# Performance work log

Measured on AMD Instinct MI355X. Metric: run time of the kernel, lower is better.

Reference implementation:

```python
import jax, jax.numpy as jnp
import numpy as np

N_NODES = 50000   # field_size == number of graph nodes
N_EDGES = 800000  # avg degree 16
VOCAB = 200000    # feature_size
EMB = 64          # embedding_size == in_dim
HID = 64          # num_hidden
SLOPE = 0.2       # leaky relu negative slope


def setup_inputs() -> dict:
    key = jax.random.key(0)
    ks = jax.random.split(key, 20)
    s = 0.05
    d = {}
    d["features"] = jax.random.randint(ks[0], (8, N_NODES), 0, VOCAB, dtype=jnp.int32)
    d["feature_values"] = jax.random.uniform(ks[1], (8, N_NODES), dtype=jnp.float32)
    d["src"] = jax.random.randint(ks[2], (N_EDGES,), 0, N_NODES, dtype=jnp.int32)
    d["dst"] = jax.random.randint(ks[3], (N_EDGES,), 0, N_NODES, dtype=jnp.int32)
    d["emb"] = jax.random.normal(ks[4], (VOCAB, EMB), jnp.float32) * s
    # layer 0: in=64 -> heads=2, out=64 (no residual)
    d["W0"]  = jax.random.normal(ks[5], (EMB, 2 * HID), jnp.float32) * s
    d["al0"] = jax.random.normal(ks[6], (2, HID), jnp.float32) * s
    d["ar0"] = jax.random.normal(ks[7], (2, HID), jnp.float32) * s
    d["b0"]  = jnp.zeros((2 * HID,), jnp.float32)
    # layer 1: in=128 -> heads=2, out=64 (identity residual since in == heads*out)
    d["W1"]  = jax.random.normal(ks[8], (2 * HID, 2 * HID), jnp.float32) * s
    d["al1"] = jax.random.normal(ks[9], (2, HID), jnp.float32) * s
    d["ar1"] = jax.random.normal(ks[10], (2, HID), jnp.float32) * s
    d["b1"]  = jnp.zeros((2 * HID,), jnp.float32)
    # output layer: in=128 -> heads=1, out=64 (projected residual), no activation
    d["W2"]    = jax.random.normal(ks[11], (2 * HID, EMB), jnp.float32) * s
    d["al2"]   = jax.random.normal(ks[12], (1, EMB), jnp.float32) * s
    d["ar2"]   = jax.random.normal(ks[13], (1, EMB), jnp.float32) * s
    d["b2"]    = jnp.zeros((EMB,), jnp.float32)
    d["resW2"] = jax.random.normal(ks[14], (2 * HID, EMB), jnp.float32) * s
    return d


def _gat_layer(h, src, dst, W, al, ar, b, res, act):
    """DGL-style GATConv. h: [N, in], W: [in, H*D], al/ar: [H, D]."""
    N = h.shape[0]
    H, D = al.shape
    fh = (h @ W).reshape(N, H, D)                      # [N, H, D]
    el = jnp.einsum('nhd,hd->nh', fh, al)              # [N, H]
    er = jnp.einsum('nhd,hd->nh', fh, ar)              # [N, H]
    e = jax.nn.leaky_relu(el[src] + er[dst], SLOPE)    # [E, H]
    # edge softmax grouped by destination node
    m = jax.ops.segment_max(e, dst, num_segments=N)
    m = jnp.where(jnp.isfinite(m), m, 0.0)
    ex = jnp.exp(e - m[dst])
    den = jax.ops.segment_sum(ex, dst, num_segments=N)
    alpha = ex / jnp.maximum(den[dst], 1e-9)           # [E, H]
    out = jax.ops.segment_sum(alpha[:, :, None] * fh[src], dst, num_segments=N)  # [N, H, D]
    if res is not None:
        out = out + res
    out = out + b.reshape(H, D)
    if act:
        out = jax.nn.elu(out)
    return out


def reference(features, feature_values, src, dst, emb,
              W0, al0, ar0, b0, W1, al1, ar1, b1,
              W2, al2, ar2, b2, resW2):
    # embedding lookup scaled by feature values: [B, field, emb]
    fe = emb[features] * feature_values[..., None]
    h = fe[0]                                          # [N_NODES, EMB]
    # layer 0: no residual, elu, flatten heads
    h = _gat_layer(h, src, dst, W0, al0, ar0, b0, None, True).reshape(N_NODES, -1)
    # layer 1: identity residual (in == heads*out), elu, flatten heads
    res1 = h.reshape(N_NODES, 2, HID)
    h = _gat_layer(h, src, dst, W1, al1, ar1, b1, res1, True).reshape(N_NODES, -1)
    # output layer: projected residual, no activation, mean over heads
    res2 = (h @ resW2).reshape(N_NODES, 1, EMB)
    logits = _gat_layer(h, src, dst, W2, al2, ar2, b2, res2, False).mean(axis=1)
    return logits
```

## Files before the change

kernel.cpp:

```cpp
#include <hip/hip_runtime.h>


typedef __attribute__((ext_vector_type(8))) short short8;
typedef __attribute__((ext_vector_type(4))) float float4v;

__device__ __forceinline__ float lrelu(float x){ return x >= 0.f ? x : 0.2f*x; }

__device__ __forceinline__ unsigned short f2bf(float f){
  unsigned int u = __float_as_uint(f);
  u += 0x7fffu + ((u >> 16) & 1u);
  return (unsigned short)(u >> 16);
}
__device__ __forceinline__ float bf2f(unsigned short u){
  return __uint_as_float((unsigned int)u << 16);
}
__device__ __forceinline__ float rl_f(float v, int l){
  return __int_as_float(__builtin_amdgcn_readlane(__float_as_int(v), l));
}

__global__ void k_zero_i32(int* __restrict__ p, int n){
  int i = blockIdx.x*blockDim.x + threadIdx.x;
  if (i < n) p[i] = 0;
}

__global__ void k_hist(const int* __restrict__ dst, int* __restrict__ counts, int E){
  int i = blockIdx.x*blockDim.x + threadIdx.x;
  if (i < E) atomicAdd(&counts[dst[i]], 1);
}

__global__ void k_scan_local(const int* __restrict__ counts, int* __restrict__ row_ptr,
                             int* __restrict__ bsum, int N){
  __shared__ int s[256];
  int t = threadIdx.x, g = blockIdx.x*256 + t;
  int v = (g < N) ? counts[g] : 0;
  s[t] = v; __syncthreads();
  #pragma unroll
  for (int off = 1; off < 256; off <<= 1){
    int x = 0;
    if (t >= off) x = s[t-off];
    __syncthreads();
    s[t] += x;
    __syncthreads();
  }
  if (g < N) row_ptr[g+1] = s[t];
  if (g == 0 && t == 0) row_ptr[0] = 0;
  if (t == 255) bsum[blockIdx.x] = s[255];
}

__global__ void k_scan_top(int* __restrict__ bsum, int nb){
  __shared__ int s[256];
  int t = threadIdx.x;
  int v = (t < nb) ? bsum[t] : 0;
  s[t] = v; __syncthreads();
  #pragma unroll
  for (int off = 1; off < 256; off <<= 1){
    int x = 0;
    if (t >= off) x = s[t-off];
    __syncthreads();
    s[t] += x;
    __syncthreads();
  }
  if (t < nb) bsum[t] = s[t] - v;
}

__global__ void k_scan_fix(int* __restrict__ row_ptr, const int* __restrict__ bsum, int N){
  int g = blockIdx.x*256 + threadIdx.x;
  if (g < N && blockIdx.x > 0) row_ptr[g+1] += bsum[blockIdx.x];
}

__global__ void k_scatter(const int* __restrict__ src, const int* __restrict__ dst,
                          const int* __restrict__ row_ptr, int* __restrict__ cursor,
                          int* __restrict__ ssrc, int E){
  int i = blockIdx.x*blockDim.x + threadIdx.x;
  if (i >= E) return;
  int d = dst[i];
  int pos = atomicAdd(&cursor[d], 1);
  ssrc[row_ptr[d] + pos] = src[i];
}

__global__ void k_wprep(const float* __restrict__ Wa, const float* __restrict__ Wb,
                        int IN, unsigned short* __restrict__ Wt){
  int id = blockIdx.x*256 + threadIdx.x;
  if (id >= 128*IN) return;
  int n = id / IN, k = id % IN;
  float v;
  if (Wb) v = (n < 64) ? Wa[k*64 + n] : Wb[k*64 + (n - 64)];
  else    v = Wa[k*128 + n];
  Wt[n*IN + k] = f2bf(v);
}

__global__ void k_embed(const int* __restrict__ feat, const float* __restrict__ fv,
                        const float* __restrict__ emb, unsigned int* __restrict__ h0b, int N){
  int t = blockIdx.x*blockDim.x + threadIdx.x;
  int n = t >> 4, c4 = t & 15;
  if (n >= N) return;
  float4 v = ((const float4*)(emb + (size_t)feat[n]*64))[c4];
  float sc = fv[n];
  unsigned int p0 = (unsigned)f2bf(v.x*sc) | ((unsigned)f2bf(v.y*sc) << 16);
  unsigned int p1 = (unsigned)f2bf(v.z*sc) | ((unsigned)f2bf(v.w*sc) << 16);
  h0b[(size_t)n*32 + c4*2]     = p0;
  h0b[(size_t)n*32 + c4*2 + 1] = p1;
}

template<int IN, int H>
__global__ __launch_bounds__(256) void k_gemm_mfma(
    const unsigned short* __restrict__ hb,
    const unsigned short* __restrict__ Wt,
    const float* __restrict__ al, const float* __restrict__ ar,
    unsigned short* __restrict__ fhb,
    float* __restrict__ elr, int N){
  constexpr int KS = IN/32;
  constexpr int LDP = IN + 8;
  __shared__ unsigned short Wt_s[128*LDP];
  const int t = threadIdx.x;
  const int lane = t & 63, wid = t >> 6;
  const int l15 = lane & 15, quad = lane >> 4;
  const int row0 = blockIdx.x*64 + wid*16;

  for (int id = t; id < 128*(IN/8); id += 256){
    int r = id/(IN/8), seg = id%(IN/8);
    ((uint4*)(Wt_s + r*LDP))[seg] = ((const uint4*)(Wt + (size_t)r*IN))[seg];
  }
  short8 a[KS];
  int arow = row0 + l15;
  #pragma unroll
  for (int s = 0; s < KS; s++){
    if (arow < N) a[s] = *(const short8*)(hb + (size_t)arow*IN + s*32 + quad*8);
    else          a[s] = short8{0,0,0,0,0,0,0,0};
  }
  __syncthreads();

  float4v acc[8];
  #pragma unroll
  for (int nt = 0; nt < 8; nt++) acc[nt] = float4v{0.f,0.f,0.f,0.f};
  #pragma unroll
  for (int nt = 0; nt < 8; nt++){
    #pragma unroll
    for (int s = 0; s < KS; s++){
      short8 b = *(const short8*)(Wt_s + (nt*16 + l15)*LDP + s*32 + quad*8);
      acc[nt] = __builtin_amdgcn_mfma_f32_16x16x32_bf16(a[s], b, acc[nt], 0, 0, 0);
    }
  }

  float alc[8], arc[8];
  #pragma unroll
  for (int nt = 0; nt < 8; nt++){
    bool hv = (H == 2) || (nt < 4);
    alc[nt] = hv ? al[nt*16 + l15] : 0.f;
    arc[nt] = hv ? ar[nt*16 + l15] : 0.f;
  }
  #pragma unroll
  for (int reg = 0; reg < 4; reg++){
    int row = row0 + quad*4 + reg;
    bool rv = row < N;
    if (rv){
      #pragma unroll
      for (int nt = 0; nt < 8; nt++)
        fhb[(size_t)row*128 + nt*16 + l15] = f2bf(acc[nt][reg]);
    }
    float pel0 = 0.f, per0 = 0.f, pel1 = 0.f, per1 = 0.f;
    #pragma unroll
    for (int nt = 0; nt < 4; nt++){
      pel0 += acc[nt][reg]*alc[nt];     per0 += acc[nt][reg]*arc[nt];
      pel1 += acc[nt+4][reg]*alc[nt+4]; per1 += acc[nt+4][reg]*arc[nt+4];
    }
    #pragma unroll
    for (int off = 1; off < 16; off <<= 1){
      pel0 += __shfl_xor(pel0, off, 64);
      pel1 += __shfl_xor(pel1, off, 64);
      per0 += __shfl_xor(per0, off, 64);
      per1 += __shfl_xor(per1, off, 64);
    }
    if (l15 == 0 && rv){
      elr[row*4+0] = pel0;
      elr[row*4+1] = (H == 2) ? pel1 : 0.f;
      elr[row*4+2] = per0;
      elr[row*4+3] = (H == 2) ? per1 : 0.f;
    }
  }
}

template<int H>
__global__ __launch_bounds__(256) void k_agg(
    const unsigned* __restrict__ fhb, const float* __restrict__ elr,
    const int* __restrict__ row_ptr, const int* __restrict__ ssrc,
    const float* __restrict__ bias, const float* __restrict__ res,
    int act, int res_from_fh,
    float* __restrict__ out, int out_ld, unsigned* __restrict__ outb, int N){
  int lane = threadIdx.x & 63, wid = threadIdx.x >> 6;
  int n = blockIdx.x*4 + wid;
  if (n >= N) return;
  int beg = row_ptr[n], end = row_ptr[n+1];
  float er0 = elr[n*4+2];
  float er1 = (H == 2) ? elr[n*4+3] : 0.f;

  float x0 = 0.f, x1 = 0.f;
  {
    int i = beg + lane;
    if (i < end){
      int s = ssrc[i];
      float2 el = *(const float2*)(elr + s*4);
      x0 = __expf(fminf(lrelu(el.x + er0), 30.f));
      if (H == 2) x1 = __expf(fminf(lrelu(el.y + er1), 30.f));
    }
  }
  float d0 = x0, d1 = x1;
  for (int i = beg + lane + 64; i < end; i += 64){
    int s = ssrc[i];
    float2 el = *(const float2*)(elr + s*4);
    d0 += __expf(fminf(lrelu(el.x + er0), 30.f));
    if (H == 2) d1 += __expf(fminf(lrelu(el.y + er1), 30.f));
  }
  #pragma unroll
  for (int off = 32; off >= 1; off >>= 1){
    d0 += __shfl_xor(d0, off, 64);
    if (H == 2) d1 += __shfl_xor(d1, off, 64);
  }
  float rd0 = d0 > 0.f ? 1.f/d0 : 0.f;
  float rd1 = (H == 2 && d1 > 0.f) ? 1.f/d1 : 0.f;

  float ax = 0.f, ay = 0.f;
  for (int base = beg; base < end; base += 64){
    int i = base + lane;
    int s = 0; float a0 = 0.f, a1 = 0.f;
    if (i < end){
      s = ssrc[i];
      if (base == beg){
        a0 = x0 * rd0; if (H == 2) a1 = x1 * rd1;
      } else {
        float2 el = *(const float2*)(elr + s*4);
        a0 = __expf(fminf(lrelu(el.x + er0), 30.f)) * rd0;
        if (H == 2) a1 = __expf(fminf(lrelu(el.y + er1), 30.f)) * rd1;
      }
    }
    int cnt  = min(64, end - base);
    int cnt8 = (cnt + 7) & ~7;
    if (H == 2){
      for (int j0 = 0; j0 < cnt8; j0 += 8){
        unsigned w[8]; float aj[8];
        #pragma unroll
        for (int u = 0; u < 8; u++){
          int sj = __builtin_amdgcn_readlane(s, j0 + u);
          w[u] = fhb[(size_t)sj*64 + lane];
        }
        #pragma unroll
        for (int u = 0; u < 8; u++){
          float aj0 = rl_f(a0, j0 + u);
          float aj1 = rl_f(a1, j0 + u);
          aj[u] = (lane < 32) ? aj0 : aj1;
        }
        #pragma unroll
        for (int u = 0; u < 8; u++){
          ax += bf2f((unsigned short)(w[u] & 0xffffu)) * aj[u];
          ay += bf2f((unsigned short)(w[u] >> 16))     * aj[u];
        }
      }
    } else {
      const unsigned short* fh16 = (const unsigned short*)fhb;
      for (int j0 = 0; j0 < cnt8; j0 += 8){
        unsigned short w[8]; float aj[8];
        #pragma unroll
        for (int u = 0; u < 8; u++){
          int sj = __builtin_amdgcn_readlane(s, j0 + u);
          w[u] = fh16[(size_t)sj*128 + lane];
        }
        #pragma unroll
        for (int u = 0; u < 8; u++) aj[u] = rl_f(a0, j0 + u);
        #pragma unroll
        for (int u = 0; u < 8; u++) ax += bf2f(w[u]) * aj[u];
      }
    }
  }
  if (H == 2){
    int c0 = lane*2;
    float o0 = ax + bias[c0], o1 = ay + bias[c0+1];
    if (res){ o0 += res[n*128 + c0]; o1 += res[n*128 + c0+1]; }
    if (act){ o0 = o0 > 0.f ? o0 : expm1f(o0); o1 = o1 > 0.f ? o1 : expm1f(o1); }
    *(float2*)(out + n*out_ld + c0) = make_float2(o0, o1);
    if (outb) outb[(size_t)n*64 + lane] = (unsigned)f2bf(o0) | ((unsigned)f2bf(o1) << 16);
  } else {
    const unsigned short* fh16 = (const unsigned short*)fhb;
    float o = ax + bias[lane];
    if (res_from_fh) o += bf2f(fh16[(size_t)n*128 + 64 + lane]);
    out[n*out_ld + lane] = o;
  }
}

extern "C" void kernel_launch(void* const* d_in, const int* in_sizes, int n_in,
                              void* d_out, int out_size, void* d_ws, size_t ws_size,
                              hipStream_t stream) {
  const int*   feat = (const int*)  d_in[0];
  const float* fv   = (const float*)d_in[1];
  const int*   src  = (const int*)  d_in[2];
  const int*   dst  = (const int*)  d_in[3];
  const float* emb  = (const float*)d_in[4];
  const float* W0   = (const float*)d_in[5];
  const float* al0  = (const float*)d_in[6];
  const float* ar0  = (const float*)d_in[7];
  const float* b0   = (const float*)d_in[8];
  const float* W1   = (const float*)d_in[9];
  const float* al1  = (const float*)d_in[10];
  const float* ar1  = (const float*)d_in[11];
  const float* b1   = (const float*)d_in[12];
  const float* W2   = (const float*)d_in[13];
  const float* al2  = (const float*)d_in[14];
  const float* ar2  = (const float*)d_in[15];
  const float* b2   = (const float*)d_in[16];
  const float* rW2  = (const float*)d_in[17];
  const int N = in_sizes[0] / 8;
  const int E = in_sizes[2];

  size_t off = 0;
  auto alloc = [&](size_t bytes) -> void* {
    void* p = (char*)d_ws + off;
    off = (off + bytes + 255) & ~(size_t)255;
    return p;
  };
  unsigned short* P1 = (unsigned short*)alloc((size_t)N*128*sizeof(unsigned short));
  float* P2     = (float*)alloc((size_t)N*128*sizeof(float));
  float* P3     = (float*)alloc((size_t)N*128*sizeof(float));
  unsigned short* hb = (unsigned short*)alloc((size_t)N*128*sizeof(unsigned short));
  float* elr    = (float*)alloc((size_t)N*4*sizeof(float));
  int* row_ptr  = (int*)alloc((size_t)(N+1)*sizeof(int));
  int* counts   = (int*)alloc((size_t)2*N*sizeof(int));
  int* cursor   = counts + N;
  int* ssrc     = (int*)alloc((size_t)E*sizeof(int));
  int* bsum     = (int*)alloc(256*sizeof(int));
  unsigned short* Wt0 = (unsigned short*)alloc((size_t)128*64*sizeof(unsigned short));
  unsigned short* Wt1 = (unsigned short*)alloc((size_t)128*128*sizeof(unsigned short));
  unsigned short* Wt2 = (unsigned short*)alloc((size_t)128*128*sizeof(unsigned short));

  int nb1 = (N + 255) / 256;
  k_zero_i32<<<(2*N + 255)/256, 256, 0, stream>>>(counts, 2*N);
  k_hist<<<(E + 255)/256, 256, 0, stream>>>(dst, counts, E);
  k_scan_local<<<nb1, 256, 0, stream>>>(counts, row_ptr, bsum, N);
  k_scan_top<<<1, 256, 0, stream>>>(bsum, nb1);
  k_scan_fix<<<nb1, 256, 0, stream>>>(row_ptr, bsum, N);
  k_scatter<<<(E + 255)/256, 256, 0, stream>>>(src, dst, row_ptr, cursor, ssrc, E);
  k_wprep<<<(128*64 + 255)/256, 256, 0, stream>>>(W0, nullptr, 64, Wt0);
  k_wprep<<<(128*128 + 255)/256, 256, 0, stream>>>(W1, nullptr, 128, Wt1);
  k_wprep<<<(128*128 + 255)/256, 256, 0, stream>>>(W2, rW2, 128, Wt2);
  k_embed<<<(N*16 + 255)/256, 256, 0, stream>>>(feat, fv, emb, (unsigned int*)hb, N);

  int gt = (N + 63)/64;
  int nagg = (N + 3)/4;
  k_gemm_mfma<64,2><<<gt, 256, 0, stream>>>(hb, Wt0, al0, ar0, P1, elr, N);
  k_agg<2><<<nagg, 256, 0, stream>>>((unsigned*)P1, elr, row_ptr, ssrc, b0, nullptr,
                                     1, 0, P2, 128, (unsigned*)hb, N);
  k_gemm_mfma<128,2><<<gt, 256, 0, stream>>>(hb, Wt1, al1, ar1, P1, elr, N);
  k_agg<2><<<nagg, 256, 0, stream>>>((unsigned*)P1, elr, row_ptr, ssrc, b1, P2,
                                     1, 0, P3, 128, (unsigned*)hb, N);
  k_gemm_mfma<128,1><<<gt, 256, 0, stream>>>(hb, Wt2, al2, ar2, P1, elr, N);
  k_agg<1><<<nagg, 256, 0, stream>>>((unsigned*)P1, elr, row_ptr, ssrc, b2, nullptr,
                                     0, 1, (float*)d_out, 64, nullptr, N);
}
```

Baseline: 368.3 us.

## Record atomic ranks during histogram, merge weight prep, use bpermute for attention broadcast

The histogram kernel now stores each edge's atomic rank, so the scatter pass indexes directly and needs no second set of atomics or cursor array. The three weight-prep launches are merged into one. In the H=2 aggregation, the per-edge attention coefficients are broadcast with ds_bpermute instead of two readlanes plus a select. The unused fp32 output of layer 1 is no longer written, and leaky ReLU becomes a branchless fmax. Together these cut atomics, launches, memory traffic and instruction count, at the cost of an extra E-sized rank buffer and reliance on LDS-permute latency.

Result: faster. 333.1 us (-9.6%).

```diff
diff --git a/kernel.cpp b/kernel.cpp
--- a/kernel.cpp
+++ b/kernel.cpp
@@ -4,7 +4,7 @@
 typedef __attribute__((ext_vector_type(8))) short short8;
 typedef __attribute__((ext_vector_type(4))) float float4v;
 
-__device__ __forceinline__ float lrelu(float x){ return x >= 0.f ? x : 0.2f*x; }
+__device__ __forceinline__ float lrelu(float x){ return fmaxf(x, 0.2f*x); }
 
 __device__ __forceinline__ unsigned short f2bf(float f){
   unsigned int u = __float_as_uint(f);
@@ -23,9 +23,13 @@
   if (i < n) p[i] = 0;
 }
 
-__global__ void k_hist(const int* __restrict__ dst, int* __restrict__ counts, int E){
+__global__ void k_hist_rank(const int* __restrict__ dst, int* __restrict__ counts,
+                            int* __restrict__ rank, int E){
   int i = blockIdx.x*blockDim.x + threadIdx.x;
-  if (i < E) atomicAdd(&counts[dst[i]], 1);
+  if (i < E){
+    int d = dst[i];
+    rank[i] = atomicAdd(&counts[d], 1);
+  }
 }
 
 __global__ void k_scan_local(const int* __restrict__ counts, int* __restrict__ row_ptr,
@@ -68,25 +72,29 @@
   if (g < N && blockIdx.x > 0) row_ptr[g+1] += bsum[blockIdx.x];
 }
 
-__global__ void k_scatter(const int* __restrict__ src, const int* __restrict__ dst,
-                          const int* __restrict__ row_ptr, int* __restrict__ cursor,
-                          int* __restrict__ ssrc, int E){
+__global__ void k_scatter2(const int* __restrict__ src, const int* __restrict__ dst,
+                           const int* __restrict__ rank, const int* __restrict__ row_ptr,
+                           int* __restrict__ ssrc, int E){
   int i = blockIdx.x*blockDim.x + threadIdx.x;
-  if (i >= E) return;
-  int d = dst[i];
-  int pos = atomicAdd(&cursor[d], 1);
-  ssrc[row_ptr[d] + pos] = src[i];
-}
-
-__global__ void k_wprep(const float* __restrict__ Wa, const float* __restrict__ Wb,
-                        int IN, unsigned short* __restrict__ Wt){
+  if (i < E) ssrc[row_ptr[dst[i]] + rank[i]] = src[i];
+}
+
+__global__ void k_wprep_all(const float* __restrict__ W0, const float* __restrict__ W1,
+                            const float* __restrict__ W2, const float* __restrict__ rW2,
+                            unsigned short* __restrict__ Wt0, unsigned short* __restrict__ Wt1,
+                            unsigned short* __restrict__ Wt2){
   int id = blockIdx.x*256 + threadIdx.x;
-  if (id >= 128*IN) return;
-  int n = id / IN, k = id % IN;
-  float v;
-  if (Wb) v = (n < 64) ? Wa[k*64 + n] : Wb[k*64 + (n - 64)];
-  else    v = Wa[k*128 + n];
-  Wt[n*IN + k] = f2bf(v);
+  if (id < 128*64){
+    int n = id/64, k = id%64;
+    Wt0[n*64 + k] = f2bf(W0[k*128 + n]);
+  } else if (id < 128*64 + 128*128){
+    int i = id - 128*64; int n = i/128, k = i%128;
+    Wt1[n*128 + k] = f2bf(W1[k*128 + n]);
+  } else if (id < 128*64 + 2*128*128){
+    int i = id - 128*64 - 128*128; int n = i/128, k = i%128;
+    float v = (n < 64) ? W2[k*64 + n] : rW2[k*64 + (n - 64)];
+    Wt2[n*128 + k] = f2bf(v);
+  }
 }
 
 __global__ void k_embed(const int* __restrict__ feat, const float* __restrict__ fv,
@@ -220,6 +228,7 @@
   float rd1 = (H == 2 && d1 > 0.f) ? 1.f/d1 : 0.f;
 
   float ax = 0.f, ay = 0.f;
+  const int idxbase = (lane & 32) << 2;
   for (int base = beg; base < end; base += 64){
     int i = base + lane;
     int s = 0; float a0 = 0.f, a1 = 0.f;
@@ -236,7 +245,13 @@
     int cnt  = min(64, end - base);
     int cnt8 = (cnt + 7) & ~7;
     if (H == 2){
+      float a1x = __shfl_xor(a1, 32, 64);
+      float a0x = __shfl_xor(a0, 32, 64);
+      int ap  = __float_as_int((lane < 32) ? a0  : a1x);
+      int ap2 = __float_as_int((lane < 32) ? a0x : a1);
       for (int j0 = 0; j0 < cnt8; j0 += 8){
+        int apx = (j0 < 32) ? ap : ap2;
+        int jb = j0 & 31;
         unsigned w[8]; float aj[8];
         #pragma unroll
         for (int u = 0; u < 8; u++){
@@ -244,11 +259,9 @@
           w[u] = fhb[(size_t)sj*64 + lane];
         }
         #pragma unroll
-        for (int u = 0; u < 8; u++){
-          float aj0 = rl_f(a0, j0 + u);
-          float aj1 = rl_f(a1, j0 + u);
-          aj[u] = (lane < 32) ? aj0 : aj1;
-        }
+        for (int u = 0; u < 8; u++)
+          aj[u] = __int_as_float(
+              __builtin_amdgcn_ds_bpermute(idxbase + ((jb + u) << 2), apx));
         #pragma unroll
         for (int u = 0; u < 8; u++){
           ax += bf2f((unsigned short)(w[u] & 0xffffu)) * aj[u];
@@ -276,7 +289,7 @@
     float o0 = ax + bias[c0], o1 = ay + bias[c0+1];
     if (res){ o0 += res[n*128 + c0]; o1 += res[n*128 + c0+1]; }
     if (act){ o0 = o0 > 0.f ? o0 : expm1f(o0); o1 = o1 > 0.f ? o1 : expm1f(o1); }
-    *(float2*)(out + n*out_ld + c0) = make_float2(o0, o1);
+    if (out) *(float2*)(out + n*out_ld + c0) = make_float2(o0, o1);
     if (outb) outb[(size_t)n*64 + lane] = (unsigned)f2bf(o0) | ((unsigned)f2bf(o1) << 16);
   } else {
     const unsigned short* fh16 = (const unsigned short*)fhb;
@@ -318,12 +331,11 @@
   };
   unsigned short* P1 = (unsigned short*)alloc((size_t)N*128*sizeof(unsigned short));
   float* P2     = (float*)alloc((size_t)N*128*sizeof(float));
-  float* P3     = (float*)alloc((size_t)N*128*sizeof(float));
   unsigned short* hb = (unsigned short*)alloc((size_t)N*128*sizeof(unsigned short));
   float* elr    = (float*)alloc((size_t)N*4*sizeof(float));
   int* row_ptr  = (int*)alloc((size_t)(N+1)*sizeof(int));
-  int* counts   = (int*)alloc((size_t)2*N*sizeof(int));
-  int* cursor   = counts + N;
+  int* counts   = (int*)alloc((size_t)N*sizeof(int));
+  int* rank     = (int*)alloc((size_t)E*sizeof(int));
   int* ssrc     = (int*)alloc((size_t)E*sizeof(int));
   int* bsum     = (int*)alloc(256*sizeof(int));
   unsigned short* Wt0 = (unsigned short*)alloc((size_t)128*64*sizeof(unsigned short));
@@ -331,15 +343,14 @@
   unsigned short* Wt2 = (unsigned short*)alloc((size_t)128*128*sizeof(unsigned short));
 
   int nb1 = (N + 255) / 256;
-  k_zero_i32<<<(2*N + 255)/256, 256, 0, stream>>>(counts, 2*N);
-  k_hist<<<(E + 255)/256, 256, 0, stream>>>(dst, counts, E);
+  k_zero_i32<<<(N + 255)/256, 256, 0, stream>>>(counts, N);
+  k_hist_rank<<<(E + 255)/256, 256, 0, stream>>>(dst, counts, rank, E);
   k_scan_local<<<nb1, 256, 0, stream>>>(counts, row_ptr, bsum, N);
   k_scan_top<<<1, 256, 0, stream>>>(bsum, nb1);
   k_scan_fix<<<nb1, 256, 0, stream>>>(row_ptr, bsum, N);
-  k_scatter<<<(E + 255)/256, 256, 0, stream>>>(src, dst, row_ptr, cursor, ssrc, E);
-  k_wprep<<<(128*64 + 255)/256, 256, 0, stream>>>(W0, nullptr, 64, Wt0);
-  k_wprep<<<(128*128 + 255)/256, 256, 0, stream>>>(W1, nullptr, 128, Wt1);
-  k_wprep<<<(128*128 + 255)/256, 256, 0, stream>>>(W2, rW2, 128, Wt2);
+  k_scatter2<<<(E + 255)/256, 256, 0, stream>>>(src, dst, rank, row_ptr, ssrc, E);
+  k_wprep_all<<<(128*64 + 2*128*128 + 255)/256, 256, 0, stream>>>(
+      W0, W1, W2, rW2, Wt0, Wt1, Wt2);
   k_embed<<<(N*16 + 255)/256, 256, 0, stream>>>(feat, fv, emb, (unsigned int*)hb, N);
 
   int gt = (N + 63)/64;
@@ -349,7 +360,7 @@
                                      1, 0, P2, 128, (unsigned*)hb, N);
   k_gemm_mfma<128,2><<<gt, 256, 0, stream>>>(hb, Wt1, al1, ar1, P1, elr, N);
   k_agg<2><<<nagg, 256, 0, stream>>>((unsigned*)P1, elr, row_ptr, ssrc, b1, P2,
-                                     1, 0, P3, 128, (unsigned*)hb, N);
+                                     1, 0, nullptr, 128, (unsigned*)hb, N);
   k_gemm_mfma<128,1><<<gt, 256, 0, stream>>>(hb, Wt2, al2, ar2, P1, elr, N);
   k_agg<1><<<nagg, 256, 0, stream>>>((unsigned*)P1, elr, row_ptr, ssrc, b2, nullptr,
                                      0, 1, (float*)d_out, 64, nullptr, N);
```
